# Optimization experiments

Hardware: AMD Instinct MI355X
Metric: run time of the kernel (lower is better)

Reference implementation:

```python
import jax, jax.numpy as jnp
import numpy as np

B, T, S, H = 8, 256, 256, 512

def setup_inputs() -> dict:
    key = jax.random.key(0)
    k1, k2, k3, k4, k5, k6 = jax.random.split(key, 6)
    query = jax.random.normal(k1, (B, T, H), dtype=jnp.float32)
    encoder_outputs = jax.random.normal(k2, (B, S, H), dtype=jnp.float32)
    # lengths in [1, S] so every row has at least one valid source position
    src_lengths = jax.random.randint(k3, (B,), 1, S + 1, dtype=jnp.int64)
    scale = 1.0 / np.sqrt(H)
    W_h = jax.random.normal(k4, (H, H), dtype=jnp.float32) * scale  # nn.Linear weight (out, in)
    W_s = jax.random.normal(k5, (H, H), dtype=jnp.float32) * scale
    v = jax.random.normal(k6, (H,), dtype=jnp.float32) * scale     # nn.Linear(H,1) weight squeezed
    return {"query": query, "encoder_outputs": encoder_outputs,
            "src_lengths": src_lengths, "W_h": W_h, "W_s": W_s, "v": v}

def reference(query, encoder_outputs, src_lengths, W_h, W_s, v):
    # Linear without bias: y = x @ W^T
    enc_f = jnp.einsum('bsh,oh->bso', encoder_outputs, W_h)   # (B,S,H)
    qry_f = jnp.einsum('bth,oh->bto', query, W_s)             # (B,T,H)
    # additive score: v^T tanh(enc_f + qry_f), broadcast over (T,S)
    scores = jnp.einsum('btsh,h->bts',
                        jnp.tanh(enc_f[:, None, :, :] + qry_f[:, :, None, :]), v)  # (B,T,S)
    mask = jnp.arange(S)[None, :] >= src_lengths[:, None]      # (B,S) True = pad
    scores = jnp.where(mask[:, None, :], -jnp.inf, scores)
    attn_weights = jax.nn.softmax(scores, axis=-1)             # (B,T,S)
    attn_out = jnp.einsum('bts,bsh->bth', attn_weights, encoder_outputs)
    return attn_out
```

## Files before the change

### kernel.cpp

```cpp
#include <hip/hip_runtime.h>
#include <cstddef>
#include <math.h>

#define BD 8
#define TD 256
#define SD 256
#define HD 512
#define K2F 2.885390081777927f

#define EXP2(x) __builtin_amdgcn_exp2f(x)
#define RCP(x)  __builtin_amdgcn_rcpf(x)

typedef __attribute__((ext_vector_type(8))) _Float16 half8;
typedef __attribute__((ext_vector_type(4))) _Float16 half4;
typedef __attribute__((ext_vector_type(4))) float float4v;

__device__ __forceinline__ float exp2_sat(float x) {
    return EXP2(fminf(fmaxf(x, -80.0f), 80.0f));
}

#define LSTR 40

__global__ __launch_bounds__(1024) void projK(
    const float* __restrict__ enc, const float* __restrict__ qry,
    const float* __restrict__ Wh,  const float* __restrict__ Ws,
    float* __restrict__ encT, float* __restrict__ qryf)
{
    __shared__ float smem[2560];

    const int bid = blockIdx.x;
    const int tid = threadIdx.x;
    const int l  = tid & 63;
    const int w  = tid >> 6;
    const int rf = l & 15;
    const int q  = l >> 4;

    _Float16* LA = (_Float16*)smem;
    _Float16* LB = (_Float16*)(smem + 1280);

    const int x  = bid & 7;
    const int k  = bid >> 3;
    const bool isq = k >= 32;
    const int kk = k & 31;
    const int my = (isq ? 32 : 0) + x * 4 + (kk & 3);
    const int n0 = (kk >> 2) * 64;
    const int m0 = my * 64;

    const bool stagesA = (tid < 512);
    const int srow = (tid >> 3) & 63;
    const int scol = (tid & 7) * 4;
    const float* Sbase = stagesA
        ? (isq ? qry + (size_t)(m0 - 2048 + srow) * HD
               : enc + (size_t)(m0 + srow) * HD) + scol
        : (isq ? Ws : Wh) + (size_t)(n0 + srow) * HD + scol;
    _Float16* Ldst = (stagesA ? LA : LB) + srow * LSTR + scol;

    const int mi = (w & 3) * 16;
    const int ni = (w >> 2) * 16;

    float4v acc = {0, 0, 0, 0};

    float4 a0 = *(const float4*)(Sbase);

    for (int ks = 0; ks < 16; ++ks) {
        if (ks) __syncthreads();
        {
            half4 ha;
            ha[0]=(_Float16)a0.x; ha[1]=(_Float16)a0.y; ha[2]=(_Float16)a0.z; ha[3]=(_Float16)a0.w;
            *(half4*)Ldst = ha;
        }
        __syncthreads();
        if (ks + 1 < 16) a0 = *(const float4*)(Sbase + (ks + 1) * 32);
        half8 ah = *(const half8*)&LA[(mi + rf) * LSTR + q * 8];
        half8 bh = *(const half8*)&LB[(ni + rf) * LSTR + q * 8];
        acc = __builtin_amdgcn_mfma_f32_16x16x32_f16(ah, bh, acc, 0, 0, 0);
    }

    if (!isq) {
        const int b  = m0 >> 8;
        const int sb = (m0 & 255) + mi + q * 4;
        float* base = encT + (size_t)b * HD * SD;
        float4 o = make_float4(exp2_sat(acc[0]*K2F), exp2_sat(acc[1]*K2F),
                               exp2_sat(acc[2]*K2F), exp2_sat(acc[3]*K2F));
        *(float4*)(base + (size_t)(n0 + ni + rf) * SD + sb) = o;
    } else {
        const int mrow = (m0 - 2048) + mi + q * 4;
        #pragma unroll
        for (int r = 0; r < 4; ++r)
            qryf[(size_t)(mrow + r) * HD + n0 + ni + rf] = exp2_sat(acc[r] * K2F);
    }
}

__global__ __launch_bounds__(1024) void attnK(
    const float* __restrict__ enc, const float* __restrict__ encT,
    const float* __restrict__ qryf, const float* __restrict__ v,
    const int* __restrict__ lens, float* __restrict__ out)
{
    __shared__ float smem[14336];

    const int bid = blockIdx.x;
    const int tid = threadIdx.x;
    const int b   = bid & 7;
    const int t0  = (bid >> 3) * 8;
    const int l = tid & 63;
    const int w = tid >> 6;

    float* qls = smem;
    float* pls = smem + 4096;
    float* wls = smem + 12288;

    {
        const float* qf = qryf + ((size_t)b * TD + t0) * HD;
        const int j = tid & 511;
        #pragma unroll
        for (int t = (tid >> 9); t < 8; t += 2)
            qls[t * 512 + j] = qf[t * HD + j];
    }
    __syncthreads();

    float a[8][4];
    #pragma unroll
    for (int t = 0; t < 8; ++t)
        #pragma unroll
        for (int c = 0; c < 4; ++c) a[t][c] = 0.0f;
    {
        const int jbase = w * 32;
        const float* ep = encT + (size_t)b * HD * SD + (size_t)jbase * SD + l * 4;
        #pragma unroll 4
        for (int jj = 0; jj < 32; ++jj) {
            float4 e = *(const float4*)(ep + (size_t)jj * SD);
            float vj = v[jbase + jj];
            float qv[8];
            #pragma unroll
            for (int t = 0; t < 8; ++t) qv[t] = qls[t * 512 + jbase + jj];
            float ev[4] = {e.x, e.y, e.z, e.w};
            #pragma unroll
            for (int t = 0; t < 8; ++t)
                #pragma unroll
                for (int c = 0; c < 4; ++c) {
                    float p = fmaf(ev[c], qv[t], 1.0f);
                    a[t][c] = fmaf(vj, RCP(p), a[t][c]);
                }
        }
    }
    if (w < 4) {
        #pragma unroll
        for (int t = 0; t < 8; ++t)
            *(float4*)&pls[(w * 8 + t) * 256 + l * 4] =
                make_float4(a[t][0], a[t][1], a[t][2], a[t][3]);
    }
    __syncthreads();
    if (w >= 4 && w < 8) {
        #pragma unroll
        for (int t = 0; t < 8; ++t) {
            float4 c4 = *(const float4*)&pls[((w - 4) * 8 + t) * 256 + l * 4];
            c4.x += a[t][0]; c4.y += a[t][1]; c4.z += a[t][2]; c4.w += a[t][3];
            *(float4*)&pls[((w - 4) * 8 + t) * 256 + l * 4] = c4;
        }
    }
    __syncthreads();
    if (w >= 8 && w < 12) {
        #pragma unroll
        for (int t = 0; t < 8; ++t) {
            float4 c4 = *(const float4*)&pls[((w - 8) * 8 + t) * 256 + l * 4];
            c4.x += a[t][0]; c4.y += a[t][1]; c4.z += a[t][2]; c4.w += a[t][3];
            *(float4*)&pls[((w - 8) * 8 + t) * 256 + l * 4] = c4;
        }
    }
    __syncthreads();
    if (w >= 12) {
        #pragma unroll
        for (int t = 0; t < 8; ++t) {
            float4 c4 = *(const float4*)&pls[((w - 12) * 8 + t) * 256 + l * 4];
            c4.x += a[t][0]; c4.y += a[t][1]; c4.z += a[t][2]; c4.w += a[t][3];
            *(float4*)&pls[((w - 12) * 8 + t) * 256 + l * 4] = c4;
        }
    }
    __syncthreads();

    if (w < 8) {
        const int t = w;
        float p[4] = {0, 0, 0, 0};
        #pragma unroll
        for (int g = 0; g < 4; ++g) {
            float4 pp = *(const float4*)&pls[(g * 8 + t) * 256 + l * 4];
            p[0] += pp.x; p[1] += pp.y; p[2] += pp.z; p[3] += pp.w;
        }
        const int len = lens[b];
        const int s0 = l * 4;
        float sc[4];
        #pragma unroll
        for (int c = 0; c < 4; ++c)
            sc[c] = (s0 + c < len) ? -2.0f * p[c] : -INFINITY;
        float mx = fmaxf(fmaxf(sc[0], sc[1]), fmaxf(sc[2], sc[3]));
        #pragma unroll
        for (int off = 32; off; off >>= 1) mx = fmaxf(mx, __shfl_xor(mx, off));
        float ex[4]; float sum = 0.0f;
        #pragma unroll
        for (int c = 0; c < 4; ++c) { ex[c] = __expf(sc[c] - mx); sum += ex[c]; }
        #pragma unroll
        for (int off = 32; off; off >>= 1) sum += __shfl_xor(sum, off);
        const float inv = RCP(sum);
        *(float4*)&wls[t * SD + s0] = make_float4(ex[0]*inv, ex[1]*inv, ex[2]*inv, ex[3]*inv);
    }
    __syncthreads();

    const int sg = tid >> 7;
    const int h4 = (tid & 127) * 4;
    float* avred = pls;
    float4 o[8];
    #pragma unroll
    for (int t = 0; t < 8; ++t) o[t] = make_float4(0.f, 0.f, 0.f, 0.f);
    {
        const float* eb = enc + (size_t)b * SD * HD + h4;
        #pragma unroll 2
        for (int ss = 0; ss < 32; ++ss) {
            const int s = sg * 32 + ss;
            float4 evv = *(const float4*)(eb + (size_t)s * HD);
            float wt[8];
            #pragma unroll
            for (int t = 0; t < 8; ++t) wt[t] = wls[t * SD + s];
            #pragma unroll
            for (int t = 0; t < 8; ++t) {
                o[t].x = fmaf(wt[t], evv.x, o[t].x);
                o[t].y = fmaf(wt[t], evv.y, o[t].y);
                o[t].z = fmaf(wt[t], evv.z, o[t].z);
                o[t].w = fmaf(wt[t], evv.w, o[t].w);
            }
        }
    }
    if (sg < 2) {
        #pragma unroll
        for (int t = 0; t < 8; ++t)
            *(float4*)&avred[(size_t)(sg * 8 + t) * 512 + h4] = o[t];
    }
    __syncthreads();
    if (sg >= 2 && sg < 4) {
        #pragma unroll
        for (int t = 0; t < 8; ++t) {
            float4 c4 = *(const float4*)&avred[(size_t)((sg - 2) * 8 + t) * 512 + h4];
            c4.x += o[t].x; c4.y += o[t].y; c4.z += o[t].z; c4.w += o[t].w;
            *(float4*)&avred[(size_t)((sg - 2) * 8 + t) * 512 + h4] = c4;
        }
    }
    __syncthreads();
    if (sg >= 4 && sg < 6) {
        #pragma unroll
        for (int t = 0; t < 8; ++t) {
            float4 c4 = *(const float4*)&avred[(size_t)((sg - 4) * 8 + t) * 512 + h4];
            c4.x += o[t].x; c4.y += o[t].y; c4.z += o[t].z; c4.w += o[t].w;
            *(float4*)&avred[(size_t)((sg - 4) * 8 + t) * 512 + h4] = c4;
        }
    }
    __syncthreads();
    if (sg >= 6) {
        #pragma unroll
        for (int t = 0; t < 8; ++t) {
            float4 c4 = *(const float4*)&avred[(size_t)((sg - 6) * 8 + t) * 512 + h4];
            c4.x += o[t].x; c4.y += o[t].y; c4.z += o[t].z; c4.w += o[t].w;
            *(float4*)&avred[(size_t)((sg - 6) * 8 + t) * 512 + h4] = c4;
        }
    }
    __syncthreads();

    {
        const int t  = tid >> 7;
        const int hh = (tid & 127) * 4;
        float4 x0 = *(const float4*)&avred[(size_t)(0 * 8 + t) * 512 + hh];
        float4 x1 = *(const float4*)&avred[(size_t)(1 * 8 + t) * 512 + hh];
        float4 r = make_float4(x0.x + x1.x, x0.y + x1.y, x0.z + x1.z, x0.w + x1.w);
        *(float4*)(out + ((size_t)b * TD + t0 + t) * HD + hh) = r;
    }
}

extern "C" void kernel_launch(void* const* d_in, const int* in_sizes, int n_in,
                              void* d_out, int out_size, void* d_ws, size_t ws_size,
                              hipStream_t stream) {
    const float* query = (const float*)d_in[0];
    const float* enc   = (const float*)d_in[1];
    const int*   lens  = (const int*)d_in[2];
    const float* W_h   = (const float*)d_in[3];
    const float* W_s   = (const float*)d_in[4];
    const float* v     = (const float*)d_in[5];
    float* out = (float*)d_out;

    char* ws = (char*)d_ws;
    float* encT = (float*)(ws);
    float* qryf = (float*)(ws + ((size_t)4 << 20));

    projK<<<dim3(512), dim3(1024), 0, stream>>>(enc, query, W_h, W_s, encT, qryf);
    attnK<<<dim3(256), dim3(1024), 0, stream>>>(enc, encT, qryf, v, lens, out);
}
```

Before: 119.1 us.

## Split attention into H-split score kernel and separate softmax/PV kernel

Replaces the single fused attention kernel with two kernels. The score kernel splits the hidden dimension in two halves across 512 blocks, writing partial score sums to workspace. A second kernel adds the partials, applies the mask and softmax, and does the weighted sum over encoder outputs with 4 query rows per block. This is meant to double the block count and improve occupancy on the score phase, at the cost of an extra launch and a round trip of partial scores through global memory. The old path is kept as a fallback when the workspace is too small.

```diff
diff --git a/kernel.cpp b/kernel.cpp
--- a/kernel.cpp
+++ b/kernel.cpp
@@ -88,6 +88,183 @@
         #pragma unroll
         for (int r = 0; r < 4; ++r)
             qryf[(size_t)(mrow + r) * HD + n0 + ni + rf] = exp2_sat(acc[r] * K2F);
+    }
+}
+
+__global__ __launch_bounds__(1024, 8) void scoreK(
+    const float* __restrict__ encT, const float* __restrict__ qryf,
+    const float* __restrict__ v, float* __restrict__ part)
+{
+    __shared__ float smem[12288];
+
+    const int bid = blockIdx.x;
+    const int tid = threadIdx.x;
+    const int b    = bid & 7;
+    const int toct = (bid >> 3) & 31;
+    const int jh   = bid >> 8;
+    const int t0   = toct * 8;
+    const int l = tid & 63;
+    const int w = tid >> 6;
+
+    float* qls = smem;
+    float* pls = smem + 4096;
+
+    {
+        const float* qf = qryf + ((size_t)b * TD + t0) * HD;
+        const int j = tid & 511;
+        #pragma unroll
+        for (int t = (tid >> 9); t < 8; t += 2)
+            qls[t * 512 + j] = qf[t * HD + j];
+    }
+    __syncthreads();
+
+    float a[8][4];
+    #pragma unroll
+    for (int t = 0; t < 8; ++t)
+        #pragma unroll
+        for (int c = 0; c < 4; ++c) a[t][c] = 0.0f;
+    {
+        const int jbase = jh * 256 + w * 16;
+        const float* ep = encT + (size_t)b * HD * SD + (size_t)jbase * SD + l * 4;
+        #pragma unroll 4
+        for (int jj = 0; jj < 16; ++jj) {
+            float4 e = *(const float4*)(ep + (size_t)jj * SD);
+            float vj = v[jbase + jj];
+            float qv[8];
+            #pragma unroll
+            for (int t = 0; t < 8; ++t) qv[t] = qls[t * 512 + jbase + jj];
+            float ev[4] = {e.x, e.y, e.z, e.w};
+            #pragma unroll
+            for (int t = 0; t < 8; ++t)
+                #pragma unroll
+                for (int c = 0; c < 4; ++c) {
+                    float p = fmaf(ev[c], qv[t], 1.0f);
+                    a[t][c] = fmaf(vj, RCP(p), a[t][c]);
+                }
+        }
+    }
+    if (w < 4) {
+        #pragma unroll
+        for (int t = 0; t < 8; ++t)
+            *(float4*)&pls[(w * 8 + t) * 256 + l * 4] =
+                make_float4(a[t][0], a[t][1], a[t][2], a[t][3]);
+    }
+    __syncthreads();
+    if (w >= 4 && w < 8) {
+        #pragma unroll
+        for (int t = 0; t < 8; ++t) {
+            float4 c4 = *(const float4*)&pls[((w - 4) * 8 + t) * 256 + l * 4];
+            c4.x += a[t][0]; c4.y += a[t][1]; c4.z += a[t][2]; c4.w += a[t][3];
+            *(float4*)&pls[((w - 4) * 8 + t) * 256 + l * 4] = c4;
+        }
+    }
+    __syncthreads();
+    if (w >= 8 && w < 12) {
+        #pragma unroll
+        for (int t = 0; t < 8; ++t) {
+            float4 c4 = *(const float4*)&pls[((w - 8) * 8 + t) * 256 + l * 4];
+            c4.x += a[t][0]; c4.y += a[t][1]; c4.z += a[t][2]; c4.w += a[t][3];
+            *(float4*)&pls[((w - 8) * 8 + t) * 256 + l * 4] = c4;
+        }
+    }
+    __syncthreads();
+    if (w >= 12) {
+        #pragma unroll
+        for (int t = 0; t < 8; ++t) {
+            float4 c4 = *(const float4*)&pls[((w - 12) * 8 + t) * 256 + l * 4];
+            c4.x += a[t][0]; c4.y += a[t][1]; c4.z += a[t][2]; c4.w += a[t][3];
+            *(float4*)&pls[((w - 12) * 8 + t) * 256 + l * 4] = c4;
+        }
+    }
+    __syncthreads();
+
+    if (w < 8) {
+        const int t = w;
+        float p[4] = {0, 0, 0, 0};
+        #pragma unroll
+        for (int g = 0; g < 4; ++g) {
+            float4 pp = *(const float4*)&pls[(g * 8 + t) * 256 + l * 4];
+            p[0] += pp.x; p[1] += pp.y; p[2] += pp.z; p[3] += pp.w;
+        }
+        *(float4*)&part[(((size_t)b * 256 + t0 + t) * 2 + jh) * 256 + l * 4] =
+            make_float4(p[0], p[1], p[2], p[3]);
+    }
+}
+
+__global__ __launch_bounds__(512) void attn2K(
+    const float* __restrict__ enc, const float* __restrict__ part,
+    const int* __restrict__ lens, float* __restrict__ out)
+{
+    __shared__ float avred[8192];
+    __shared__ float wls[4 * SD];
+
+    const int bid = blockIdx.x;
+    const int tid = threadIdx.x;
+    const int b   = bid & 7;
+    const int t0  = (bid >> 3) * 4;
+    const int w   = tid >> 6;
+    const int l   = tid & 63;
+
+    if (w < 4) {
+        const int t = w;
+        const int s0 = l * 4;
+        const float* pb = part + (((size_t)b * 256 + t0 + t) * 2) * 256 + s0;
+        float4 h0 = *(const float4*)(pb);
+        float4 h1 = *(const float4*)(pb + 256);
+        float p[4] = {h0.x + h1.x, h0.y + h1.y, h0.z + h1.z, h0.w + h1.w};
+        const int len = lens[b];
+        float sc[4];
+        #pragma unroll
+        for (int c = 0; c < 4; ++c)
+            sc[c] = (s0 + c < len) ? -2.0f * p[c] : -INFINITY;
+        float mx = fmaxf(fmaxf(sc[0], sc[1]), fmaxf(sc[2], sc[3]));
+        #pragma unroll
+        for (int off = 32; off; off >>= 1) mx = fmaxf(mx, __shfl_xor(mx, off));
+        float ex[4]; float sum = 0.0f;
+        #pragma unroll
+        for (int c = 0; c < 4; ++c) { ex[c] = __expf(sc[c] - mx); sum += ex[c]; }
+        #pragma unroll
+        for (int off = 32; off; off >>= 1) sum += __shfl_xor(sum, off);
+        const float inv = RCP(sum);
+        *(float4*)&wls[t * SD + s0] = make_float4(ex[0]*inv, ex[1]*inv, ex[2]*inv, ex[3]*inv);
+    }
+    __syncthreads();
+
+    const int g  = tid >> 7;
+    const int h4 = (tid & 127) * 4;
+    {
+        const float* eb = enc + (size_t)b * SD * HD + h4;
+        float4 o[4] = {{0,0,0,0},{0,0,0,0},{0,0,0,0},{0,0,0,0}};
+        #pragma unroll 2
+        for (int ss = 0; ss < 64; ++ss) {
+            const int s = g * 64 + ss;
+            float4 evv = *(const float4*)(eb + (size_t)s * HD);
+            float wt[4];
+            #pragma unroll
+            for (int t = 0; t < 4; ++t) wt[t] = wls[t * SD + s];
+            #pragma unroll
+            for (int t = 0; t < 4; ++t) {
+                o[t].x = fmaf(wt[t], evv.x, o[t].x);
+                o[t].y = fmaf(wt[t], evv.y, o[t].y);
+                o[t].z = fmaf(wt[t], evv.z, o[t].z);
+                o[t].w = fmaf(wt[t], evv.w, o[t].w);
+            }
+        }
+        #pragma unroll
+        for (int t = 0; t < 4; ++t)
+            *(float4*)&avred[(size_t)(g * 4 + t) * 512 + h4] = o[t];
+    }
+    __syncthreads();
+    {
+        const int t  = tid >> 7;
+        const int hh = (tid & 127) * 4;
+        float4 r = {0, 0, 0, 0};
+        #pragma unroll
+        for (int gg = 0; gg < 4; ++gg) {
+            float4 x = *(const float4*)&avred[(size_t)(gg * 4 + t) * 512 + hh];
+            r.x += x.x; r.y += x.y; r.z += x.z; r.w += x.w;
+        }
+        *(float4*)(out + ((size_t)b * TD + t0 + t) * HD + hh) = r;
     }
 }
 
@@ -287,7 +464,14 @@
     char* ws = (char*)d_ws;
     float* encT = (float*)(ws);
     float* qryf = (float*)(ws + ((size_t)4 << 20));
+    float* part = (float*)(ws + ((size_t)8 << 20));
 
     projK<<<dim3(512), dim3(1024), 0, stream>>>(enc, query, W_h, W_s, encT, qryf);
-    attnK<<<dim3(256), dim3(1024), 0, stream>>>(enc, encT, qryf, v, lens, out);
-}
+
+    if (ws_size >= ((size_t)12 << 20)) {
+        scoreK<<<dim3(512), dim3(1024), 0, stream>>>(encT, qryf, v, part);
+        attn2K<<<dim3(512), dim3(512),  0, stream>>>(enc, part, lens, out);
+    } else {
+        attnK<<<dim3(256), dim3(1024), 0, stream>>>(enc, encT, qryf, v, lens, out);
+    }
+}
```

Result: slower. 257.3 us (+116.0%).
